# Performance work log

Measured on AMD Instinct MI355X. Metric: run time of the kernel, lower is better.

## Reference

```python
import jax, jax.numpy as jnp
import numpy as np

B, C, H, W, E, HEADS = 8, 128, 96, 96, 16, 4
HD = C // HEADS

def _ln(x, g, b, eps=1e-5):
    m = jnp.mean(x, axis=-1, keepdims=True)
    v = jnp.mean(jnp.square(x - m), axis=-1, keepdims=True)
    return (x - m) * jax.lax.rsqrt(v + eps) * g + b

def _gelu(x):
    return jax.nn.gelu(x, approximate=False)  # torch nn.GELU default (erf)

def setup_inputs() -> dict:
    key = jax.random.key(0)
    ks = iter(jax.random.split(key, 48))
    def wgt(shape, s=0.02):
        return jax.random.normal(next(ks), shape, jnp.float32) * s
    d = {
        "feature_map": jax.random.normal(next(ks), (B, C, H, W), jnp.float32),
        "hyperedge_scores": jax.random.uniform(next(ks), (B, H * W, E), jnp.float32),
        # norm_node_pre
        "np_g": jnp.ones((C,), jnp.float32), "np_b": jnp.zeros((C,), jnp.float32),
        # MultiheadAttention (self-attn over hyperedges)
        "mha_w_in": wgt((3 * C, C)), "mha_b_in": jnp.zeros((3 * C,), jnp.float32),
        "mha_w_out": wgt((C, C)), "mha_b_out": jnp.zeros((C,), jnp.float32),
        # transformer FFN
        "ffn_w1": wgt((2 * C, C)), "ffn_b1": jnp.zeros((2 * C,), jnp.float32),
        "ffn_w2": wgt((C, 2 * C)), "ffn_b2": jnp.zeros((C,), jnp.float32),
        # shared LayerNorm inside HypergraphTransformerConv (used twice)
        "tnorm_g": jnp.ones((C,), jnp.float32), "tnorm_b": jnp.zeros((C,), jnp.float32),
        # norm_hyper
        "nh_g": jnp.ones((C,), jnp.float32), "nh_b": jnp.zeros((C,), jnp.float32),
        # hyper_proj
        "hp_w": wgt((C, C)), "hp_b": jnp.zeros((C,), jnp.float32),
        # HyperedgeGuidedNodeAttention
        "q_w": wgt((C, C)), "q_b": jnp.zeros((C,), jnp.float32),
        "kv_w": wgt((2 * C, C)), "kv_b": jnp.zeros((2 * C,), jnp.float32),
        # norm_fusion
        "nf_g": jnp.ones((2 * C,), jnp.float32), "nf_b": jnp.zeros((2 * C,), jnp.float32),
        # gate = Linear(2C->C) + LayerNorm(C) + Sigmoid
        "gate_w": wgt((C, 2 * C)), "gate_b": jnp.zeros((C,), jnp.float32),
        "gate_ln_g": jnp.ones((C,), jnp.float32), "gate_ln_b": jnp.zeros((C,), jnp.float32),
        # node_proj
        "nproj_w": wgt((C, C)), "nproj_b": jnp.zeros((C,), jnp.float32),
    }
    return d

def _forward(feature_map, hyperedge_scores, np_g, np_b, mha_w_in, mha_b_in,
             mha_w_out, mha_b_out, ffn_w1, ffn_b1, ffn_w2, ffn_b2,
             tnorm_g, tnorm_b, nh_g, nh_b, hp_w, hp_b, q_w, q_b, kv_w, kv_b,
             nf_g, nf_b, gate_w, gate_b, gate_ln_g, gate_ln_b, nproj_w, nproj_b):
    b, c, h, w = feature_map.shape
    n = h * w
    node = jnp.transpose(feature_map.reshape(b, c, n), (0, 2, 1))   # [B,N,C]
    node = _ln(node, np_g, np_b)
    # hyperedge aggregation: H^T @ X -> [B,E,C]
    hyper = jnp.einsum('bne,bnc->bec', hyperedge_scores, node)
    # --- HypergraphTransformerConv (self-attn over E=16 hyperedges) ---
    qkv = hyper @ mha_w_in.T + mha_b_in                               # [B,E,3C]
    q, k, v = jnp.split(qkv, 3, axis=-1)
    def heads(x):  # [B,E,C] -> [B,h,E,hd]
        return jnp.transpose(x.reshape(b, E, HEADS, HD), (0, 2, 1, 3))
    q, k, v = heads(q), heads(k), heads(v)
    attn = jax.nn.softmax(jnp.einsum('bhqd,bhkd->bhqk', q, k) / np.sqrt(HD), axis=-1)
    ao = jnp.einsum('bhqk,bhkd->bhqd', attn, v)
    ao = jnp.transpose(ao, (0, 2, 1, 3)).reshape(b, E, c)
    ao = ao @ mha_w_out.T + mha_b_out
    x = _ln(hyper + ao, tnorm_g, tnorm_b)
    ffn = _gelu(x @ ffn_w1.T + ffn_b1) @ ffn_w2.T + ffn_b2
    hyper = _ln(x + ffn, tnorm_g, tnorm_b)
    # ---
    hyper = _ln(hyper, nh_g, nh_b)
    hyper = _gelu(hyper @ hp_w.T + hp_b)                              # [B,E,C]
    intra = jnp.einsum('bne,bec->bnc', hyperedge_scores, hyper)       # [B,N,C]
    # HyperedgeGuidedNodeAttention (scale = C**-0.5)
    Q = node @ q_w.T + q_b
    K, V = jnp.split(hyper @ kv_w.T + kv_b, 2, axis=-1)
    a = jax.nn.softmax(jnp.einsum('bnc,bec->bne', Q, K) * (c ** -0.5), axis=-1)
    cross = jnp.einsum('bne,bec->bnc', a, V)
    combined = _ln(jnp.concatenate([intra, cross], axis=-1), nf_g, nf_b)
    gate = jax.nn.sigmoid(_ln(combined @ gate_w.T + gate_b, gate_ln_g, gate_ln_b))
    fused = gate * intra + (1.0 - gate) * cross
    upd = node + fused                                                # dropout in eval mode
    out = _gelu(upd @ nproj_w.T + nproj_b)
    return jnp.transpose(out, (0, 2, 1)).reshape(b, c, h, w)

def reference(feature_map, hyperedge_scores, np_g, np_b, mha_w_in, mha_b_in,
              mha_w_out, mha_b_out, ffn_w1, ffn_b1, ffn_w2, ffn_b2,
              tnorm_g, tnorm_b, nh_g, nh_b, hp_w, hp_b, q_w, q_b, kv_w, kv_b,
              nf_g, nf_b, gate_w, gate_b, gate_ln_g, gate_ln_b, nproj_w, nproj_b):
    return _forward(feature_map, hyperedge_scores, np_g, np_b, mha_w_in, mha_b_in,
                    mha_w_out, mha_b_out, ffn_w1, ffn_b1, ffn_w2, ffn_b2,
                    tnorm_g, tnorm_b, nh_g, nh_b, hp_w, hp_b, q_w, q_b, kv_w, kv_b,
                    nf_g, nf_b, gate_w, gate_b, gate_ln_g, gate_ln_b, nproj_w, nproj_b)
```

## Files before the change

### kernel.cpp

```cpp
#include <hip/hip_runtime.h>

typedef unsigned short bf_t;
typedef unsigned int u32;
typedef short short8 __attribute__((ext_vector_type(8)));
typedef float f32x4 __attribute__((ext_vector_type(4)));

#define NB 8
#define CC 128
#define NN 9216
#define EE 16

__device__ __forceinline__ float b2f(bf_t u){ return __uint_as_float(((u32)u)<<16); }
__device__ __forceinline__ bf_t f2b(float f){
  u32 u = __float_as_uint(f);
  u = (u + 0x7fffu + ((u>>16)&1u)) >> 16;
  return (bf_t)u;
}
__device__ __forceinline__ float gelu_f(float x){ return 0.5f*x*(1.f+erff(x*0.70710678118654752f)); }
__device__ __forceinline__ float red16(float v){
  #pragma unroll
  for (int m=1;m<16;m<<=1) v += __shfl_xor(v, m, 16);
  return v;
}
__device__ __forceinline__ float grs(float var){
  return rsqrtf(fmaxf(var + 1e-5f, 1e-8f));
}
__device__ __forceinline__ short8 ldw8(const float* __restrict__ p){
  float4 a = *(const float4*)p;
  float4 b = *(const float4*)(p+4);
  short8 o;
  o[0]=(short)f2b(a.x); o[1]=(short)f2b(a.y); o[2]=(short)f2b(a.z); o[3]=(short)f2b(a.w);
  o[4]=(short)f2b(b.x); o[5]=(short)f2b(b.y); o[6]=(short)f2b(b.z); o[7]=(short)f2b(b.w);
  return o;
}

template<int PRE>
__global__ __launch_bounds__(256) void k_pre(float* __restrict__ hacc,
                                             const float* __restrict__ gw,
                                             const float* __restrict__ npw,
                                             bf_t* __restrict__ gwb,
                                             bf_t* __restrict__ npwb){
  int i = blockIdx.x*256 + threadIdx.x;
  hacc[i] = 0.f;
  if (PRE){
    gwb[i]       = f2b(gw[i]);
    gwb[i+16384] = f2b(gw[i+16384]);
    npwb[i]      = f2b(npw[i]);
  }
}

__global__ __launch_bounds__(256) void k_ln_agg(const float* __restrict__ fm,
                                                const float* __restrict__ g,
                                                const float* __restrict__ bb,
                                                const float* __restrict__ sc,
                                                float* __restrict__ nln,
                                                float* __restrict__ hacc){
  int b = blockIdx.y, n0 = blockIdx.x*64, tid = threadIdx.x;
  __shared__ float xs[128*65];
  __shared__ float scs[64][17];
  __shared__ float ps[4][64], pq[4][64], mrs[2][64];
  const float* base = fm + (size_t)b*CC*NN + n0;
  #pragma unroll
  for (int p=0;p<8;p++){
    int idx = tid + p*256;
    int c = idx>>4, n4 = (idx&15)*4;
    float4 v = *(const float4*)(base + (size_t)c*NN + n4);
    xs[c*65 + n4+0] = v.x; xs[c*65 + n4+1] = v.y;
    xs[c*65 + n4+2] = v.z; xs[c*65 + n4+3] = v.w;
  }
  { int n = tid>>2, e4 = (tid&3)*4;
    float4 sv = *(const float4*)(sc + ((size_t)(b*NN + n0 + n))*EE + e4);
    scs[n][e4+0] = sv.x; scs[n][e4+1] = sv.y;
    scs[n][e4+2] = sv.z; scs[n][e4+3] = sv.w;
  }
  __syncthreads();
  { int cg = tid>>6, n = tid&63;
    float s=0.f, q=0.f;
    #pragma unroll
    for (int c=0;c<32;c++){ float v = xs[(cg*32+c)*65 + n]; s+=v; q+=v*v; }
    ps[cg][n]=s; pq[cg][n]=q;
  }
  __syncthreads();
  if (tid < 64){
    float S = ps[0][tid]+ps[1][tid]+ps[2][tid]+ps[3][tid];
    float Q = pq[0][tid]+pq[1][tid]+pq[2][tid]+pq[3][tid];
    float m = S*(1.f/128.f);
    mrs[0][tid] = m; mrs[1][tid] = grs(Q*(1.f/128.f) - m*m);
  }
  __syncthreads();
  #pragma unroll
  for (int p=0;p<8;p++){
    int idx = tid + p*256;
    int c = idx>>4, n4 = (idx&15)*4;
    float gv = g[c], bv = bb[c];
    float4 o;
    float v0 = (xs[c*65+n4+0]-mrs[0][n4+0])*mrs[1][n4+0]*gv + bv;
    float v1 = (xs[c*65+n4+1]-mrs[0][n4+1])*mrs[1][n4+1]*gv + bv;
    float v2 = (xs[c*65+n4+2]-mrs[0][n4+2])*mrs[1][n4+2]*gv + bv;
    float v3 = (xs[c*65+n4+3]-mrs[0][n4+3])*mrs[1][n4+3]*gv + bv;
    o.x=v0; o.y=v1; o.z=v2; o.w=v3;
    xs[c*65+n4+0]=v0; xs[c*65+n4+1]=v1; xs[c*65+n4+2]=v2; xs[c*65+n4+3]=v3;
    *(float4*)(nln + ((size_t)(b*CC + c))*NN + n0 + n4) = o;
  }
  __syncthreads();
  { int cp = tid&63, eh = tid>>6;
    float a0[4]={0,0,0,0}, a1[4]={0,0,0,0};
    for (int n=0;n<64;n++){
      float x0 = xs[cp*65 + n], x1 = xs[(cp+64)*65 + n];
      #pragma unroll
      for (int j=0;j<4;j++){
        float se = scs[n][eh*4+j];
        a0[j] += se*x0; a1[j] += se*x1;
      }
    }
    #pragma unroll
    for (int j=0;j<4;j++){
      float* hb = hacc + (size_t)(b*EE + eh*4 + j)*CC;
      atomicAdd(hb + cp, a0[j]);
      atomicAdd(hb + cp + 64, a1[j]);
    }
  }
}

template<int K, int NOUT, int ACT>
__device__ __forceinline__ void gemm16(const bf_t* A, int SA,
                                       const float* __restrict__ W,
                                       const float* __restrict__ bias,
                                       bf_t* O, int SO, int tid){
  int lane = tid&63, wid = tid>>6;
  int m16 = lane&15, quad = lane>>4;
  #pragma unroll
  for (int u=0; u<NOUT/64; u++){
    int n0 = u*64 + wid*16;
    f32x4 acc = {0.f,0.f,0.f,0.f};
    #pragma unroll
    for (int k0=0;k0<K;k0+=32){
      short8 af = *(const short8*)(A + m16*SA + k0 + quad*8);
      short8 bfv = ldw8(W + (size_t)(n0+m16)*K + k0 + quad*8);
      acc = __builtin_amdgcn_mfma_f32_16x16x32_bf16(af, bfv, acc, 0, 0, 0);
    }
    int col = n0 + m16;
    float bv = bias[col];
    #pragma unroll
    for (int r=0;r<4;r++){
      float v = acc[r] + bv;
      if (ACT) v = gelu_f(v);
      O[(quad*4+r)*SO + col] = f2b(v);
    }
  }
}

#define SP1 136
#define SP2 264
#define SP3 392

__global__ __launch_bounds__(256) void k_edge(const float* __restrict__ hacc,
    const float* w_in, const float* b_in, const float* w_out, const float* b_out,
    const float* w1, const float* b1, const float* w2, const float* b2v,
    const float* tg, const float* tb, const float* nhg, const float* nhb,
    const float* hpw, const float* hpb, const float* kvw, const float* kvbias,
    const float* qw, const float* qb,
    bf_t* __restrict__ hfw, bf_t* __restrict__ vws,
    bf_t* __restrict__ Ktgb, float* __restrict__ qbK){
  __shared__ __align__(16) bf_t hyp0[16*SP1];
  __shared__ __align__(16) bf_t qkvb[16*SP3];
  __shared__ __align__(16) bf_t aob [16*SP1];
  __shared__ __align__(16) bf_t xnb [16*SP1];
  __shared__ __align__(16) bf_t h1b [16*SP2];
  __shared__ __align__(16) bf_t t2b [16*SP1];
  __shared__ __align__(16) bf_t hfb [16*SP1];
  __shared__ __align__(16) bf_t kvo [16*SP2];
  int b = blockIdx.x, tid = threadIdx.x;
  int lane = tid&63, wid = tid>>6, m16 = lane&15, quad = lane>>4;

  #pragma unroll
  for (int p=0;p<8;p++){
    int idx = tid + p*256;
    int e = idx>>7, c = idx&127;
    hyp0[e*SP1 + c] = f2b(hacc[(size_t)(b*EE + e)*CC + c]);
  }
  __syncthreads();
  gemm16<128,384,0>(hyp0, SP1, w_in, b_in, qkvb, SP3, tid);
  __syncthreads();
  {
    int part = tid&3, hq = tid>>2;
    int h = hq>>4, qi = hq&15;
    int dbase = h*32 + part*8;
    float qv[8];
    #pragma unroll
    for (int j=0;j<8;j++) qv[j] = b2f(qkvb[qi*SP3 + dbase + j]);
    float dot[16];
    #pragma unroll
    for (int kk=0;kk<16;kk++){
      float s = 0.f;
      #pragma unroll
      for (int j=0;j<8;j++) s += qv[j]*b2f(qkvb[kk*SP3 + 128 + dbase + j]);
      dot[kk] = s;
    }
    #pragma unroll
    for (int m=1;m<4;m<<=1){
      #pragma unroll
      for (int kk=0;kk<16;kk++) dot[kk] += __shfl_xor(dot[kk], m, 4);
    }
    const float sc1 = 0.17677669529663687f;
    float mx = -1e30f;
    #pragma unroll
    for (int kk=0;kk<16;kk++){ dot[kk] *= sc1; mx = fmaxf(mx, dot[kk]); }
    float sum = 0.f;
    #pragma unroll
    for (int kk=0;kk<16;kk++){ dot[kk] = __expf(dot[kk]-mx); sum += dot[kk]; }
    float inv = 1.f/sum;
    float ao[8] = {0,0,0,0,0,0,0,0};
    #pragma unroll
    for (int kk=0;kk<16;kk++){
      float p = dot[kk]*inv;
      #pragma unroll
      for (int j=0;j<8;j++) ao[j] += p*b2f(qkvb[kk*SP3 + 256 + dbase + j]);
    }
    #pragma unroll
    for (int j=0;j<8;j++) aob[qi*SP1 + dbase + j] = f2b(ao[j]);
  }
  __syncthreads();
  gemm16<128,128,0>(aob, SP1, w_out, b_out, xnb, SP1, tid);
  __syncthreads();
  {
    int e = tid>>4, i = tid&15;
    float v[8]; float s=0.f, q=0.f;
    #pragma unroll
    for (int j=0;j<8;j++){
      int c = i*8+j;
      v[j] = b2f(hyp0[e*SP1+c]) + b2f(xnb[e*SP1+c]);
      s += v[j]; q += v[j]*v[j];
    }
    s = red16(s); q = red16(q);
    float m = s*(1.f/128.f);
    float rs = grs(q*(1.f/128.f) - m*m);
    #pragma unroll
    for (int j=0;j<8;j++){
      int c = i*8+j;
      xnb[e*SP1+c] = f2b((v[j]-m)*rs*tg[c] + tb[c]);
    }
  }
  __syncthreads();
  gemm16<128,256,1>(xnb, SP1, w1, b1, h1b, SP2, tid);
  __syncthreads();
  gemm16<256,128,0>(h1b, SP2, w2, b2v, aob, SP1, tid);
  __syncthreads();
  {
    int e = tid>>4, i = tid&15;
    float v[8]; float s=0.f, q=0.f;
    #pragma unroll
    for (int j=0;j<8;j++){
      int c = i*8+j;
      v[j] = b2f(xnb[e*SP1+c]) + b2f(aob[e*SP1+c]);
      s += v[j]; q += v[j]*v[j];
    }
    s = red16(s); q = red16(q);
    float m = s*(1.f/128.f);
    float rs = grs(q*(1.f/128.f) - m*m);
    float s2=0.f, q2=0.f;
    #pragma unroll
    for (int j=0;j<8;j++){
      int c = i*8+j;
      v[j] = (v[j]-m)*rs*tg[c] + tb[c];
      s2 += v[j]; q2 += v[j]*v[j];
    }
    s2 = red16(s2); q2 = red16(q2);
    float m2 = s2*(1.f/128.f);
    float rs2 = grs(q2*(1.f/128.f) - m2*m2);
    #pragma unroll
    for (int j=0;j<8;j++){
      int c = i*8+j;
      t2b[e*SP1+c] = f2b((v[j]-m2)*rs2*nhg[c] + nhb[c]);
    }
  }
  __syncthreads();
  gemm16<128,128,1>(t2b, SP1, hpw, hpb, hfb, SP1, tid);
  __syncthreads();
  gemm16<128,256,0>(hfb, SP1, kvw, kvbias, kvo, SP2, tid);
  __syncthreads();
  #pragma unroll
  for (int p=0;p<8;p++){
    int idx = tid + p*256;
    int e = idx>>7, c = idx&127;
    size_t o = (size_t)(b*EE + e)*CC + c;
    hfw[o] = hfb[e*SP1 + c];
    vws[o] = kvo[e*SP2 + 128 + c];
  }
  #pragma unroll
  for (int u=0;u<2;u++){
    int n0 = u*64 + wid*16;
    f32x4 acc = {0.f,0.f,0.f,0.f};
    #pragma unroll
    for (int k0=0;k0<128;k0+=32){
      short8 a = *(const short8*)(kvo + m16*SP2 + k0 + quad*8);
      short8 bq;
      #pragma unroll
      for (int j=0;j<8;j++)
        bq[j] = (short)f2b(qw[(size_t)(k0+quad*8+j)*128 + n0+m16]);
      acc = __builtin_amdgcn_mfma_f32_16x16x32_bf16(a, bq, acc, 0, 0, 0);
    }
    #pragma unroll
    for (int r=0;r<4;r++)
      Ktgb[(size_t)(b*EE + quad*4 + r)*CC + n0 + m16] = f2b(acc[r]);
  }
  { int e = tid>>4, i = tid&15;
    float s = 0.f;
    #pragma unroll
    for (int j=0;j<8;j++) s += qb[i*8+j]*b2f(kvo[e*SP2 + i*8+j]);
    s = red16(s);
    if (i == 0) qbK[b*EE + e] = s;
  }
}

template<int PRE>
__global__ __launch_bounds__(256,3) void k_meganode(
    float* __restrict__ io, const float* __restrict__ sc,
    const bf_t* __restrict__ hf, const bf_t* __restrict__ vw,
    const bf_t* __restrict__ ktg, const float* __restrict__ qbK,
    const float* __restrict__ nfg, const float* __restrict__ nfb,
    const float* __restrict__ gw, const bf_t* __restrict__ gwb,
    const float* __restrict__ gb,
    const float* __restrict__ glng, const float* __restrict__ glnb,
    const float* __restrict__ npw, const bf_t* __restrict__ npwb,
    const float* __restrict__ npb){
  int tid = threadIdx.x, lane = tid&63, wid = tid>>6;
  int m16 = lane&15, quad = lane>>4;
  int b = blockIdx.y, n0 = blockIdx.x*64;
  __shared__ __align__(16) char sm[49408];
  bf_t* xt  = (bf_t*)(sm);
  bf_t* ktT = (bf_t*)(sm + 17408);
  bf_t* ct  = (bf_t*)(sm + 21760);
  bf_t* hfT = (bf_t*)(sm + 39168);
  bf_t* vfT = (bf_t*)(sm + 43264);
  bf_t* ash = (bf_t*)(sm + 47360);
  float* ot = (float*)(sm);
  const short8 z8 = {0,0,0,0,0,0,0,0};

  #pragma unroll
  for (int p=0;p<8;p++){
    int idx = tid + p*256;
    int c = idx>>4, n4 = (idx&15)*4;
    float4 v = *(const float4*)(io + ((size_t)(b*CC + c))*NN + n0 + n4);
    xt[(n4+0)*136 + c] = f2b(v.x);
    xt[(n4+1)*136 + c] = f2b(v.y);
    xt[(n4+2)*136 + c] = f2b(v.z);
    xt[(n4+3)*136 + c] = f2b(v.w);
  }
  { const u32* kp = (const u32*)(ktg + (size_t)b*EE*CC);
    #pragma unroll
    for (int p=0;p<4;p++){
      int idx = tid + p*256;
      int e = idx>>6, c2 = (idx&63)*2;
      *(u32*)&ktT[e*136 + c2] = kp[idx];
    }
  }
  { const u32* hs = (const u32*)(hf + (size_t)b*EE*CC);
    const u32* vs = (const u32*)(vw + (size_t)b*EE*CC);
    #pragma unroll
    for (int p=0;p<4;p++){
      int idx = tid + p*256;
      int e = idx>>6, c2 = (idx&63)*2;
      u32 hv = hs[idx], vv = vs[idx];
      hfT[(c2+0)*16 + e] = (bf_t)(hv&0xffffu);
      hfT[(c2+1)*16 + e] = (bf_t)(hv>>16);
      vfT[(c2+0)*16 + e] = (bf_t)(vv&0xffffu);
      vfT[(c2+1)*16 + e] = (bf_t)(vv>>16);
    }
  }
  __syncthreads();

  f32x4 dacc = {0.f,0.f,0.f,0.f};
  #pragma unroll
  for (int kk=0;kk<4;kk++){
    short8 a = *(const short8*)(xt + (wid*16+m16)*136 + kk*32 + quad*8);
    short8 bfr = *(const short8*)(ktT + m16*136 + kk*32 + quad*8);
    dacc = __builtin_amdgcn_mfma_f32_16x16x32_bf16(a, bfr, dacc, 0, 0, 0);
  }
  { float qbe = qbK[b*EE + m16];
    #pragma unroll
    for (int r=0;r<4;r++){
      float v = (dacc[r] + qbe) * 0.08838834764831845f;
      float m = v;
      #pragma unroll
      for (int msk=1;msk<16;msk<<=1) m = fmaxf(m, __shfl_xor(m, msk, 16));
      float ex = __expf(v - m);
      float s = ex;
      #pragma unroll
      for (int msk=1;msk<16;msk<<=1) s += __shfl_xor(s, msk, 16);
      ash[(wid*16 + quad*4 + r)*16 + m16] = f2b(ex / s);
    }
  }

  short8 scf = z8, asf = z8;
  if (quad < 2){
    const float* sp = sc + ((size_t)(b*NN + n0 + wid*16 + m16))*EE + quad*8;
    float4 u0 = *(const float4*)sp;
    float4 u1 = *(const float4*)(sp+4);
    scf[0]=(short)f2b(u0.x); scf[1]=(short)f2b(u0.y); scf[2]=(short)f2b(u0.z); scf[3]=(short)f2b(u0.w);
    scf[4]=(short)f2b(u1.x); scf[5]=(short)f2b(u1.y); scf[6]=(short)f2b(u1.z); scf[7]=(short)f2b(u1.w);
    asf = *(const short8*)(ash + (wid*16+m16)*16 + quad*8);
  }
  f32x4 acc_it[8], acc_cr[8];
  #pragma unroll
  for (int t=0;t<8;t++){
    short8 bh = z8, bv = z8;
    if (quad < 2){
      bh = *(const short8*)(hfT + (t*16+m16)*16 + quad*8);
      bv = *(const short8*)(vfT + (t*16+m16)*16 + quad*8);
    }
    f32x4 zf = {0.f,0.f,0.f,0.f};
    acc_it[t] = __builtin_amdgcn_mfma_f32_16x16x32_bf16(scf, bh, zf, 0, 0, 0);
    acc_cr[t] = __builtin_amdgcn_mfma_f32_16x16x32_bf16(asf, bv, zf, 0, 0, 0);
  }

  float mean4[4], rstd4[4];
  { float s4[4]={0,0,0,0}, q4[4]={0,0,0,0};
    #pragma unroll
    for (int t=0;t<8;t++)
      #pragma unroll
      for (int r=0;r<4;r++){
        float a = acc_it[t][r], c = acc_cr[t][r];
        s4[r] += a + c; q4[r] += a*a + c*c;
      }
    #pragma unroll
    for (int r=0;r<4;r++){
      s4[r] = red16(s4[r]); q4[r] = red16(q4[r]);
      mean4[r] = s4[r]*(1.f/256.f);
      rstd4[r] = grs(q4[r]*(1.f/256.f) - mean4[r]*mean4[r]);
    }
  }
  short8 af[8];
  #pragma unroll
  for (int r=0;r<4;r++){
    int node = wid*16 + quad*4 + r;
    #pragma unroll
    for (int t=0;t<8;t++){
      int ch = t*16 + m16;
      ct[node*136 + ch] = f2b((acc_it[t][r]-mean4[r])*rstd4[r]*nfg[ch] + nfb[ch]);
    }
  }
  #pragma unroll
  for (int kk=0;kk<4;kk++)
    af[kk] = *(const short8*)(ct + (wid*16+m16)*136 + kk*32 + quad*8);
  #pragma unroll
  for (int r=0;r<4;r++){
    int node = wid*16 + quad*4 + r;
    #pragma unroll
    for (int t=0;t<8;t++){
      int ch = t*16 + m16;
      ct[node*136 + ch] = f2b((acc_cr[t][r]-mean4[r])*rstd4[r]*nfg[128+ch] + nfb[128+ch]);
    }
  }
  #pragma unroll
  for (int kk=0;kk<4;kk++)
    af[4+kk] = *(const short8*)(ct + (wid*16+m16)*136 + kk*32 + quad*8);

  f32x4 acc_g[8];
  #pragma unroll
  for (int t=0;t<8;t++){
    f32x4 a = {0.f,0.f,0.f,0.f};
    #pragma unroll
    for (int kk=0;kk<8;kk++){
      short8 w8 = PRE ? *(const short8*)(gwb + (size_t)(t*16+m16)*256 + kk*32 + quad*8)
                      : ldw8(gw + (size_t)(t*16+m16)*256 + kk*32 + quad*8);
      a = __builtin_amdgcn_mfma_f32_16x16x32_bf16(af[kk], w8, a, 0, 0, 0);
    }
    acc_g[t] = a;
  }

  { float s2[4]={0,0,0,0}, q2[4]={0,0,0,0};
    #pragma unroll
    for (int t=0;t<8;t++){
      float bv = gb[t*16+m16];
      #pragma unroll
      for (int r=0;r<4;r++){
        float v = acc_g[t][r] + bv;
        acc_g[t][r] = v; s2[r] += v; q2[r] += v*v;
      }
    }
    #pragma unroll
    for (int r=0;r<4;r++){ s2[r] = red16(s2[r]); q2[r] = red16(q2[r]); }
    #pragma unroll
    for (int t=0;t<8;t++){
      int col = t*16 + m16;
      float lg = glng[col], lb = glnb[col];
      #pragma unroll
      for (int r=0;r<4;r++){
        float m2 = s2[r]*(1.f/128.f);
        float rs2 = grs(q2[r]*(1.f/128.f) - m2*m2);
        float z = (acc_g[t][r]-m2)*rs2*lg + lb;
        float gs = 1.f/(1.f + __expf(-z));
        int node = wid*16 + quad*4 + r;
        float nld = b2f(xt[node*136 + col]);
        xt[node*136 + col] = f2b(nld + gs*acc_it[t][r] + (1.f-gs)*acc_cr[t][r]);
      }
    }
  }

  short8 bfu[4];
  #pragma unroll
  for (int kk=0;kk<4;kk++)
    bfu[kk] = *(const short8*)(xt + (wid*16+m16)*136 + kk*32 + quad*8);
  __syncthreads();
  #pragma unroll
  for (int mt=0;mt<8;mt++){
    f32x4 o = {0.f,0.f,0.f,0.f};
    #pragma unroll
    for (int kk=0;kk<4;kk++){
      short8 aw = PRE ? *(const short8*)(npwb + (size_t)(mt*16+m16)*128 + kk*32 + quad*8)
                      : ldw8(npw + (size_t)(mt*16+m16)*128 + kk*32 + quad*8);
      o = __builtin_amdgcn_mfma_f32_16x16x32_bf16(aw, bfu[kk], o, 0, 0, 0);
    }
    #pragma unroll
    for (int r=0;r<4;r++){
      int cp = mt*16 + quad*4 + r;
      ot[cp*68 + wid*16 + m16] = gelu_f(o[r] + npb[cp]);
    }
  }
  __syncthreads();
  #pragma unroll
  for (int p=0;p<8;p++){
    int idx = tid + p*256;
    int c = idx>>4, n4 = (idx&15)*4;
    float4 v = *(const float4*)&ot[c*68 + n4];
    *(float4*)(io + ((size_t)(b*CC + c))*NN + n0 + n4) = v;
  }
}

extern "C" void kernel_launch(void* const* d_in, const int* in_sizes, int n_in,
                              void* d_out, int out_size, void* d_ws, size_t ws_size,
                              hipStream_t stream){
  (void)in_sizes; (void)n_in; (void)out_size;
  const float* fm   = (const float*)d_in[0];
  const float* sc   = (const float*)d_in[1];
  const float* npg  = (const float*)d_in[2];
  const float* npb_ = (const float*)d_in[3];
  const float* w_in = (const float*)d_in[4];
  const float* b_in = (const float*)d_in[5];
  const float* w_out= (const float*)d_in[6];
  const float* b_out= (const float*)d_in[7];
  const float* w1   = (const float*)d_in[8];
  const float* b1   = (const float*)d_in[9];
  const float* w2   = (const float*)d_in[10];
  const float* b2v  = (const float*)d_in[11];
  const float* tg   = (const float*)d_in[12];
  const float* tb   = (const float*)d_in[13];
  const float* nhg  = (const float*)d_in[14];
  const float* nhb  = (const float*)d_in[15];
  const float* hpw  = (const float*)d_in[16];
  const float* hpb  = (const float*)d_in[17];
  const float* qw   = (const float*)d_in[18];
  const float* qb   = (const float*)d_in[19];
  const float* kvw  = (const float*)d_in[20];
  const float* kvb  = (const float*)d_in[21];
  const float* nfg  = (const float*)d_in[22];
  const float* nfb  = (const float*)d_in[23];
  const float* gw   = (const float*)d_in[24];
  const float* gb   = (const float*)d_in[25];
  const float* glng = (const float*)d_in[26];
  const float* glnb = (const float*)d_in[27];
  const float* npw  = (const float*)d_in[28];
  const float* npb2 = (const float*)d_in[29];

  float* nln = (float*)d_out;

  char* w = (char*)d_ws;
  float* hacc = (float*)(w);
  float* qbK  = (float*)(w + 65536);
  bf_t*  hfw  = (bf_t*) (w + 66048);
  bf_t*  vws  = (bf_t*) (w + 98816);
  bf_t*  Ktgb = (bf_t*) (w + 131584);
  bf_t*  gwb  = (bf_t*) (w + 164352);
  bf_t*  npwb = (bf_t*) (w + 229888);
  bool pre = (ws_size >= (size_t)262656);

  if (pre) k_pre<1><<<dim3(64), dim3(256), 0, stream>>>(hacc, gw, npw, gwb, npwb);
  else     k_pre<0><<<dim3(64), dim3(256), 0, stream>>>(hacc, gw, npw, gwb, npwb);
  k_ln_agg<<<dim3(144,8), dim3(256), 0, stream>>>(fm, npg, npb_, sc, nln, hacc);
  k_edge  <<<dim3(8),     dim3(256), 0, stream>>>(hacc, w_in,b_in,w_out,b_out,
                                                  w1,b1,w2,b2v, tg,tb, nhg,nhb,
                                                  hpw,hpb, kvw,kvb, qw,qb,
                                                  hfw, vws, Ktgb, qbK);
  if (pre)
    k_meganode<1><<<dim3(144,8), dim3(256), 0, stream>>>(nln, sc, hfw, vws, Ktgb, qbK,
                                                         nfg, nfb, gw, gwb, gb,
                                                         glng, glnb, npw, npwb, npb2);
  else
    k_meganode<0><<<dim3(144,8), dim3(256), 0, stream>>>(nln, sc, hfw, vws, Ktgb, qbK,
                                                         nfg, nfb, gw, gwb, gb,
                                                         glng, glnb, npw, npwb, npb2);
}
```

Before: 295.1 us.

## Stage node LN output as bf16 workspace and pre-convert edge-stage weights

When the workspace is large enough, the LayerNorm kernel writes a node-major bf16 copy of the normalized features to the workspace instead of fp32 channel-major output. The mega node kernel then loads that copy with vector loads and no transpose or conversion, which roughly halves read traffic. All edge-stage weights, including a transposed q weight, are also converted to bf16 once in the prep kernel, and shared memory is trimmed by aliasing ct onto ktT so more blocks fit per CU (launch bounds raised to 4). The cost is an extra 18MB workspace buffer and reliance on a large ws_size being provided.

```diff
diff --git a/kernel.cpp b/kernel.cpp
--- a/kernel.cpp
+++ b/kernel.cpp
@@ -34,27 +34,48 @@
   return o;
 }
 
-template<int PRE>
+template<int MODE>
 __global__ __launch_bounds__(256) void k_pre(float* __restrict__ hacc,
-                                             const float* __restrict__ gw,
-                                             const float* __restrict__ npw,
-                                             bf_t* __restrict__ gwb,
-                                             bf_t* __restrict__ npwb){
+    const float* __restrict__ gw, const float* __restrict__ npw,
+    bf_t* __restrict__ gwb, bf_t* __restrict__ npwb,
+    const float* __restrict__ w_in, const float* __restrict__ w_out,
+    const float* __restrict__ w1, const float* __restrict__ w2,
+    const float* __restrict__ hpw, const float* __restrict__ kvw,
+    const float* __restrict__ qw,
+    bf_t* __restrict__ w_in_b, bf_t* __restrict__ w_out_b,
+    bf_t* __restrict__ w1_b, bf_t* __restrict__ w2_b,
+    bf_t* __restrict__ hpw_b, bf_t* __restrict__ kvw_b,
+    bf_t* __restrict__ qwT_b){
   int i = blockIdx.x*256 + threadIdx.x;
   hacc[i] = 0.f;
-  if (PRE){
+  if (MODE >= 1){
     gwb[i]       = f2b(gw[i]);
     gwb[i+16384] = f2b(gw[i+16384]);
     npwb[i]      = f2b(npw[i]);
   }
-}
-
-__global__ __launch_bounds__(256) void k_ln_agg(const float* __restrict__ fm,
-                                                const float* __restrict__ g,
-                                                const float* __restrict__ bb,
-                                                const float* __restrict__ sc,
-                                                float* __restrict__ nln,
-                                                float* __restrict__ hacc){
+  if (MODE == 2){
+    #pragma unroll
+    for (int k=0;k<3;k++) w_in_b[i + k*16384] = f2b(w_in[i + k*16384]);
+    w_out_b[i]       = f2b(w_out[i]);
+    w1_b[i]          = f2b(w1[i]);
+    w1_b[i+16384]    = f2b(w1[i+16384]);
+    w2_b[i]          = f2b(w2[i]);
+    w2_b[i+16384]    = f2b(w2[i+16384]);
+    hpw_b[i]         = f2b(hpw[i]);
+    kvw_b[i]         = f2b(kvw[i]);
+    kvw_b[i+16384]   = f2b(kvw[i+16384]);
+    qwT_b[i]         = f2b(qw[(i&127)*128 + (i>>7)]);
+  }
+}
+
+template<int BFOUT>
+__global__ __launch_bounds__(256,4) void k_ln_agg(const float* __restrict__ fm,
+                                                  const float* __restrict__ g,
+                                                  const float* __restrict__ bb,
+                                                  const float* __restrict__ sc,
+                                                  float* __restrict__ nln,
+                                                  bf_t* __restrict__ nlnb,
+                                                  float* __restrict__ hacc){
   int b = blockIdx.y, n0 = blockIdx.x*64, tid = threadIdx.x;
   __shared__ float xs[128*65];
   __shared__ float scs[64][17];
@@ -93,16 +114,28 @@
     int idx = tid + p*256;
     int c = idx>>4, n4 = (idx&15)*4;
     float gv = g[c], bv = bb[c];
-    float4 o;
     float v0 = (xs[c*65+n4+0]-mrs[0][n4+0])*mrs[1][n4+0]*gv + bv;
     float v1 = (xs[c*65+n4+1]-mrs[0][n4+1])*mrs[1][n4+1]*gv + bv;
     float v2 = (xs[c*65+n4+2]-mrs[0][n4+2])*mrs[1][n4+2]*gv + bv;
     float v3 = (xs[c*65+n4+3]-mrs[0][n4+3])*mrs[1][n4+3]*gv + bv;
-    o.x=v0; o.y=v1; o.z=v2; o.w=v3;
     xs[c*65+n4+0]=v0; xs[c*65+n4+1]=v1; xs[c*65+n4+2]=v2; xs[c*65+n4+3]=v3;
-    *(float4*)(nln + ((size_t)(b*CC + c))*NN + n0 + n4) = o;
-  }
-  __syncthreads();
+    if (!BFOUT){
+      float4 o; o.x=v0; o.y=v1; o.z=v2; o.w=v3;
+      *(float4*)(nln + ((size_t)(b*CC + c))*NN + n0 + n4) = o;
+    }
+  }
+  __syncthreads();
+  if (BFOUT){
+    #pragma unroll
+    for (int p=0;p<4;p++){
+      int idx = tid + p*256;
+      int n = idx>>4, c8 = (idx&15)*8;
+      short8 o;
+      #pragma unroll
+      for (int j=0;j<8;j++) o[j] = (short)f2b(xs[(c8+j)*65 + n]);
+      *(short8*)(nlnb + ((size_t)(b*NN + n0 + n))*CC + c8) = o;
+    }
+  }
   { int cp = tid&63, eh = tid>>6;
     float a0[4]={0,0,0,0}, a1[4]={0,0,0,0};
     for (int n=0;n<64;n++){
@@ -122,9 +155,10 @@
   }
 }
 
-template<int K, int NOUT, int ACT>
+template<int K, int NOUT, int ACT, int WB>
 __device__ __forceinline__ void gemm16(const bf_t* A, int SA,
                                        const float* __restrict__ W,
+                                       const bf_t* __restrict__ Wb,
                                        const float* __restrict__ bias,
                                        bf_t* O, int SO, int tid){
   int lane = tid&63, wid = tid>>6;
@@ -136,7 +170,8 @@
     #pragma unroll
     for (int k0=0;k0<K;k0+=32){
       short8 af = *(const short8*)(A + m16*SA + k0 + quad*8);
-      short8 bfv = ldw8(W + (size_t)(n0+m16)*K + k0 + quad*8);
+      short8 bfv = WB ? *(const short8*)(Wb + (size_t)(n0+m16)*K + k0 + quad*8)
+                      : ldw8(W + (size_t)(n0+m16)*K + k0 + quad*8);
       acc = __builtin_amdgcn_mfma_f32_16x16x32_bf16(af, bfv, acc, 0, 0, 0);
     }
     int col = n0 + m16;
@@ -154,12 +189,17 @@
 #define SP2 264
 #define SP3 392
 
+template<int WB>
 __global__ __launch_bounds__(256) void k_edge(const float* __restrict__ hacc,
     const float* w_in, const float* b_in, const float* w_out, const float* b_out,
     const float* w1, const float* b1, const float* w2, const float* b2v,
     const float* tg, const float* tb, const float* nhg, const float* nhb,
     const float* hpw, const float* hpb, const float* kvw, const float* kvbias,
     const float* qw, const float* qb,
+    const bf_t* __restrict__ w_in_b, const bf_t* __restrict__ w_out_b,
+    const bf_t* __restrict__ w1_b, const bf_t* __restrict__ w2_b,
+    const bf_t* __restrict__ hpw_b, const bf_t* __restrict__ kvw_b,
+    const bf_t* __restrict__ qwT_b,
     bf_t* __restrict__ hfw, bf_t* __restrict__ vws,
     bf_t* __restrict__ Ktgb, float* __restrict__ qbK){
   __shared__ __align__(16) bf_t hyp0[16*SP1];
@@ -180,7 +220,7 @@
     hyp0[e*SP1 + c] = f2b(hacc[(size_t)(b*EE + e)*CC + c]);
   }
   __syncthreads();
-  gemm16<128,384,0>(hyp0, SP1, w_in, b_in, qkvb, SP3, tid);
+  gemm16<128,384,0,WB>(hyp0, SP1, w_in, w_in_b, b_in, qkvb, SP3, tid);
   __syncthreads();
   {
     int part = tid&3, hq = tid>>2;
@@ -221,7 +261,7 @@
     for (int j=0;j<8;j++) aob[qi*SP1 + dbase + j] = f2b(ao[j]);
   }
   __syncthreads();
-  gemm16<128,128,0>(aob, SP1, w_out, b_out, xnb, SP1, tid);
+  gemm16<128,128,0,WB>(aob, SP1, w_out, w_out_b, b_out, xnb, SP1, tid);
   __syncthreads();
   {
     int e = tid>>4, i = tid&15;
@@ -242,9 +282,9 @@
     }
   }
   __syncthreads();
-  gemm16<128,256,1>(xnb, SP1, w1, b1, h1b, SP2, tid);
-  __syncthreads();
-  gemm16<256,128,0>(h1b, SP2, w2, b2v, aob, SP1, tid);
+  gemm16<128,256,1,WB>(xnb, SP1, w1, w1_b, b1, h1b, SP2, tid);
+  __syncthreads();
+  gemm16<256,128,0,WB>(h1b, SP2, w2, w2_b, b2v, aob, SP1, tid);
   __syncthreads();
   {
     int e = tid>>4, i = tid&15;
@@ -275,9 +315,9 @@
     }
   }
   __syncthreads();
-  gemm16<128,128,1>(t2b, SP1, hpw, hpb, hfb, SP1, tid);
-  __syncthreads();
-  gemm16<128,256,0>(hfb, SP1, kvw, kvbias, kvo, SP2, tid);
+  gemm16<128,128,1,WB>(t2b, SP1, hpw, hpw_b, hpb, hfb, SP1, tid);
+  __syncthreads();
+  gemm16<128,256,0,WB>(hfb, SP1, kvw, kvw_b, kvbias, kvo, SP2, tid);
   __syncthreads();
   #pragma unroll
   for (int p=0;p<8;p++){
@@ -295,9 +335,13 @@
     for (int k0=0;k0<128;k0+=32){
       short8 a = *(const short8*)(kvo + m16*SP2 + k0 + quad*8);
       short8 bq;
-      #pragma unroll
-      for (int j=0;j<8;j++)
-        bq[j] = (short)f2b(qw[(size_t)(k0+quad*8+j)*128 + n0+m16]);
+      if (WB){
+        bq = *(const short8*)(qwT_b + (size_t)(n0+m16)*128 + k0 + quad*8);
+      } else {
+        #pragma unroll
+        for (int j=0;j<8;j++)
+          bq[j] = (short)f2b(qw[(size_t)(k0+quad*8+j)*128 + n0+m16]);
+      }
       acc = __builtin_amdgcn_mfma_f32_16x16x32_bf16(a, bq, acc, 0, 0, 0);
     }
     #pragma unroll
@@ -313,9 +357,10 @@
   }
 }
 
-template<int PRE>
-__global__ __launch_bounds__(256,3) void k_meganode(
-    float* __restrict__ io, const float* __restrict__ sc,
+template<int MODE>
+__global__ __launch_bounds__(256,4) void k_meganode(
+    float* __restrict__ io, const bf_t* __restrict__ nlnb,
+    const float* __restrict__ sc,
     const bf_t* __restrict__ hf, const bf_t* __restrict__ vw,
     const bf_t* __restrict__ ktg, const float* __restrict__ qbK,
     const float* __restrict__ nfg, const float* __restrict__ nfb,
@@ -327,25 +372,35 @@
   int tid = threadIdx.x, lane = tid&63, wid = tid>>6;
   int m16 = lane&15, quad = lane>>4;
   int b = blockIdx.y, n0 = blockIdx.x*64;
-  __shared__ __align__(16) char sm[49408];
+  __shared__ __align__(16) char sm[34816];
   bf_t* xt  = (bf_t*)(sm);
   bf_t* ktT = (bf_t*)(sm + 17408);
-  bf_t* ct  = (bf_t*)(sm + 21760);
-  bf_t* hfT = (bf_t*)(sm + 39168);
-  bf_t* vfT = (bf_t*)(sm + 43264);
-  bf_t* ash = (bf_t*)(sm + 47360);
+  bf_t* hfT = (bf_t*)(sm + 21760);
+  bf_t* vfT = (bf_t*)(sm + 25856);
+  bf_t* ash = (bf_t*)(sm + 29952);
+  bf_t* ct  = (bf_t*)(sm + 17408);
   float* ot = (float*)(sm);
   const short8 z8 = {0,0,0,0,0,0,0,0};
 
-  #pragma unroll
-  for (int p=0;p<8;p++){
-    int idx = tid + p*256;
-    int c = idx>>4, n4 = (idx&15)*4;
-    float4 v = *(const float4*)(io + ((size_t)(b*CC + c))*NN + n0 + n4);
-    xt[(n4+0)*136 + c] = f2b(v.x);
-    xt[(n4+1)*136 + c] = f2b(v.y);
-    xt[(n4+2)*136 + c] = f2b(v.z);
-    xt[(n4+3)*136 + c] = f2b(v.w);
+  if (MODE == 2){
+    const bf_t* nb = nlnb + ((size_t)(b*NN + n0))*CC;
+    #pragma unroll
+    for (int p=0;p<4;p++){
+      int idx = tid + p*256;
+      int n = idx>>4, c8 = (idx&15)*8;
+      *(short8*)&xt[n*136 + c8] = *(const short8*)(nb + (size_t)n*CC + c8);
+    }
+  } else {
+    #pragma unroll
+    for (int p=0;p<8;p++){
+      int idx = tid + p*256;
+      int c = idx>>4, n4 = (idx&15)*4;
+      float4 v = *(const float4*)(io + ((size_t)(b*CC + c))*NN + n0 + n4);
+      xt[(n4+0)*136 + c] = f2b(v.x);
+      xt[(n4+1)*136 + c] = f2b(v.y);
+      xt[(n4+2)*136 + c] = f2b(v.z);
+      xt[(n4+3)*136 + c] = f2b(v.w);
+    }
   }
   { const u32* kp = (const u32*)(ktg + (size_t)b*EE*CC);
     #pragma unroll
@@ -430,6 +485,7 @@
       rstd4[r] = grs(q4[r]*(1.f/256.f) - mean4[r]*mean4[r]);
     }
   }
+  __syncthreads();
   short8 af[8];
   #pragma unroll
   for (int r=0;r<4;r++){
@@ -462,8 +518,8 @@
     f32x4 a = {0.f,0.f,0.f,0.f};
     #pragma unroll
     for (int kk=0;kk<8;kk++){
-      short8 w8 = PRE ? *(const short8*)(gwb + (size_t)(t*16+m16)*256 + kk*32 + quad*8)
-                      : ldw8(gw + (size_t)(t*16+m16)*256 + kk*32 + quad*8);
+      short8 w8 = (MODE >= 1) ? *(const short8*)(gwb + (size_t)(t*16+m16)*256 + kk*32 + quad*8)
+                              : ldw8(gw + (size_t)(t*16+m16)*256 + kk*32 + quad*8);
       a = __builtin_amdgcn_mfma_f32_16x16x32_bf16(af[kk], w8, a, 0, 0, 0);
     }
     acc_g[t] = a;
@@ -508,8 +564,8 @@
     f32x4 o = {0.f,0.f,0.f,0.f};
     #pragma unroll
     for (int kk=0;kk<4;kk++){
-      short8 aw = PRE ? *(const short8*)(npwb + (size_t)(mt*16+m16)*128 + kk*32 + quad*8)
-                      : ldw8(npw + (size_t)(mt*16+m16)*128 + kk*32 + quad*8);
+      short8 aw = (MODE >= 1) ? *(const short8*)(npwb + (size_t)(mt*16+m16)*128 + kk*32 + quad*8)
+                              : ldw8(npw + (size_t)(mt*16+m16)*128 + kk*32 + quad*8);
       o = __builtin_amdgcn_mfma_f32_16x16x32_bf16(aw, bfu[kk], o, 0, 0, 0);
     }
     #pragma unroll
@@ -566,28 +622,56 @@
   float* nln = (float*)d_out;
 
   char* w = (char*)d_ws;
-  float* hacc = (float*)(w);
-  float* qbK  = (float*)(w + 65536);
-  bf_t*  hfw  = (bf_t*) (w + 66048);
-  bf_t*  vws  = (bf_t*) (w + 98816);
-  bf_t*  Ktgb = (bf_t*) (w + 131584);
-  bf_t*  gwb  = (bf_t*) (w + 164352);
-  bf_t*  npwb = (bf_t*) (w + 229888);
-  bool pre = (ws_size >= (size_t)262656);
-
-  if (pre) k_pre<1><<<dim3(64), dim3(256), 0, stream>>>(hacc, gw, npw, gwb, npwb);
-  else     k_pre<0><<<dim3(64), dim3(256), 0, stream>>>(hacc, gw, npw, gwb, npwb);
-  k_ln_agg<<<dim3(144,8), dim3(256), 0, stream>>>(fm, npg, npb_, sc, nln, hacc);
-  k_edge  <<<dim3(8),     dim3(256), 0, stream>>>(hacc, w_in,b_in,w_out,b_out,
-                                                  w1,b1,w2,b2v, tg,tb, nhg,nhb,
-                                                  hpw,hpb, kvw,kvb, qw,qb,
-                                                  hfw, vws, Ktgb, qbK);
-  if (pre)
-    k_meganode<1><<<dim3(144,8), dim3(256), 0, stream>>>(nln, sc, hfw, vws, Ktgb, qbK,
-                                                         nfg, nfb, gw, gwb, gb,
-                                                         glng, glnb, npw, npwb, npb2);
-  else
-    k_meganode<0><<<dim3(144,8), dim3(256), 0, stream>>>(nln, sc, hfw, vws, Ktgb, qbK,
-                                                         nfg, nfb, gw, gwb, gb,
-                                                         glng, glnb, npw, npwb, npb2);
-}
+  float* hacc    = (float*)(w);
+  float* qbK     = (float*)(w + 65536);
+  bf_t*  hfw     = (bf_t*) (w + 66048);
+  bf_t*  vws     = (bf_t*) (w + 98816);
+  bf_t*  Ktgb    = (bf_t*) (w + 131584);
+  bf_t*  gwb     = (bf_t*) (w + 164352);
+  bf_t*  npwb    = (bf_t*) (w + 229888);
+  bf_t*  w_in_b  = (bf_t*) (w + 262656);
+  bf_t*  w_out_b = (bf_t*) (w + 360960);
+  bf_t*  w1_b    = (bf_t*) (w + 393728);
+  bf_t*  w2_b    = (bf_t*) (w + 459264);
+  bf_t*  hpw_b   = (bf_t*) (w + 524800);
+  bf_t*  kvw_b   = (bf_t*) (w + 557568);
+  bf_t*  qwT_b   = (bf_t*) (w + 623104);
+  bf_t*  nlnb    = (bf_t*) (w + 655872);
+  bool full = (ws_size >= (size_t)19530240);
+  bool pre  = (ws_size >= (size_t)262656);
+
+  if (full){
+    k_pre<2><<<dim3(64), dim3(256), 0, stream>>>(hacc, gw, npw, gwb, npwb,
+        w_in, w_out, w1, w2, hpw, kvw, qw,
+        w_in_b, w_out_b, w1_b, w2_b, hpw_b, kvw_b, qwT_b);
+    k_ln_agg<1><<<dim3(144,8), dim3(256), 0, stream>>>(fm, npg, npb_, sc, nln, nlnb, hacc);
+    k_edge<1><<<dim3(8), dim3(256), 0, stream>>>(hacc, w_in,b_in,w_out,b_out,
+        w1,b1,w2,b2v, tg,tb, nhg,nhb, hpw,hpb, kvw,kvb, qw,qb,
+        w_in_b, w_out_b, w1_b, w2_b, hpw_b, kvw_b, qwT_b,
+        hfw, vws, Ktgb, qbK);
+    k_meganode<2><<<dim3(144,8), dim3(256), 0, stream>>>(nln, nlnb, sc, hfw, vws, Ktgb, qbK,
+        nfg, nfb, gw, gwb, gb, glng, glnb, npw, npwb, npb2);
+  } else if (pre){
+    k_pre<1><<<dim3(64), dim3(256), 0, stream>>>(hacc, gw, npw, gwb, npwb,
+        w_in, w_out, w1, w2, hpw, kvw, qw,
+        w_in_b, w_out_b, w1_b, w2_b, hpw_b, kvw_b, qwT_b);
+    k_ln_agg<0><<<dim3(144,8), dim3(256), 0, stream>>>(fm, npg, npb_, sc, nln, nlnb, hacc);
+    k_edge<0><<<dim3(8), dim3(256), 0, stream>>>(hacc, w_in,b_in,w_out,b_out,
+        w1,b1,w2,b2v, tg,tb, nhg,nhb, hpw,hpb, kvw,kvb, qw,qb,
+        w_in_b, w_out_b, w1_b, w2_b, hpw_b, kvw_b, qwT_b,
+        hfw, vws, Ktgb, qbK);
+    k_meganode<1><<<dim3(144,8), dim3(256), 0, stream>>>(nln, nlnb, sc, hfw, vws, Ktgb, qbK,
+        nfg, nfb, gw, gwb, gb, glng, glnb, npw, npwb, npb2);
+  } else {
+    k_pre<0><<<dim3(64), dim3(256), 0, stream>>>(hacc, gw, npw, gwb, npwb,
+        w_in, w_out, w1, w2, hpw, kvw, qw,
+        w_in_b, w_out_b, w1_b, w2_b, hpw_b, kvw_b, qwT_b);
+    k_ln_agg<0><<<dim3(144,8), dim3(256), 0, stream>>>(fm, npg, npb_, sc, nln, nlnb, hacc);
+    k_edge<0><<<dim3(8), dim3(256), 0, stream>>>(hacc, w_in,b_in,w_out,b_out,
+        w1,b1,w2,b2v, tg,tb, nhg,nhb, hpw,hpb, kvw,kvb, qw,qb,
+        w_in_b, w_out_b, w1_b, w2_b, hpw_b, kvw_b, qwT_b,
+        hfw, vws, Ktgb, qbK);
+    k_meganode<0><<<dim3(144,8), dim3(256), 0, stream>>>(nln, nlnb, sc, hfw, vws, Ktgb, qbK,
+        nfg, nfb, gw, gwb, gb, glng, glnb, npw, npwb, npb2);
+  }
+}
```

Result: no change. 298.3 us (+1.1%).
